# Kernel tuning notes

Measured on AMD Instinct MI355X. Metric: run time of the kernel, lower is better.

The kernel has to match this reference:

```python
import jax, jax.numpy as jnp
import numpy as np

# AmplitudeEncoder(num_modes=14, num_photons=4, UNBUNCHED, return_sv=False)
D = 1001  # math.comb(14, 4): statevector dimension


def setup_inputs() -> dict:
    key = jax.random.key(0)
    x = jax.random.normal(key, (64, 784), dtype=jnp.float32)
    return {"x": x}


def reference(x) -> jnp.ndarray:
    # flatten any trailing dims (already 2D here)
    B = x.shape[0]
    x = x.reshape(B, -1)
    F = x.shape[1]
    # pad features into a length-D statevector: state[:F] = features, rest zeros
    state = jnp.pad(x, ((0, 0), (0, D - F)))  # [B, D]
    # L2-normalize each sample's statevector (padding contributes 0 to the norm)
    state = state / jnp.linalg.norm(state, axis=1, keepdims=True)
    # density matrix: outer(state, conj(state)); input is real so conj is identity.
    # (original casts to complex128; values are identical for real features)
    return state[:, :, None] * state[:, None, :]  # [B, D, D]
```

## Files before the change

### kernel.cpp

```cpp
#include <hip/hip_runtime.h>


#define BATCH 64
#define F 784
#define D 1001
#define DD (D * D)
#define TOTAL (BATCH * DD)
#define TOTAL4 (TOTAL / 4)

typedef float vfloat4 __attribute__((ext_vector_type(4)));

__global__ __launch_bounds__(256) void amp_norm_kernel(
    const float* __restrict__ x, float* __restrict__ s) {
  const int b = blockIdx.x;
  const int t = threadIdx.x;
  const float* xb = x + b * F;

  float v0 = (t < F)       ? xb[t]       : 0.f;
  float v1 = (t + 256 < F) ? xb[t + 256] : 0.f;
  float v2 = (t + 512 < F) ? xb[t + 512] : 0.f;
  float v3 = (t + 768 < F) ? xb[t + 768] : 0.f;

  float sum = v0 * v0 + v1 * v1 + v2 * v2 + v3 * v3;

  #pragma unroll
  for (int off = 32; off > 0; off >>= 1)
    sum += __shfl_down(sum, off, 64);

  __shared__ float wsum[4];
  __shared__ float inv_s;
  const int wave = t >> 6;
  const int lane = t & 63;
  if (lane == 0) wsum[wave] = sum;
  __syncthreads();
  if (t == 0) {
    float tot = wsum[0] + wsum[1] + wsum[2] + wsum[3];
    inv_s = 1.0f / sqrtf(tot);
  }
  __syncthreads();
  const float inv = inv_s;

  float* sb = s + b * F;
  if (t < F)       sb[t]       = v0 * inv;
  if (t + 256 < F) sb[t + 256] = v1 * inv;
  if (t + 512 < F) sb[t + 512] = v2 * inv;
  if (t + 768 < F) sb[t + 768] = v3 * inv;
}

__global__ __launch_bounds__(256) void amp_outer_kernel(
    const float* __restrict__ s, float* __restrict__ out) {
  const unsigned int f4 = blockIdx.x * 256u + threadIdx.x;
  if (f4 >= (unsigned int)TOTAL4) return;
  const unsigned int f = f4 * 4u;

  unsigned int bb = f / (unsigned int)DD;
  unsigned int rem = f - bb * (unsigned int)DD;
  unsigned int ii = rem / (unsigned int)D;
  unsigned int jj = rem - ii * (unsigned int)D;

  float r = (ii < F) ? s[bb * F + ii] : 0.f;

  float vals[4];
  #pragma unroll
  for (int k = 0; k < 4; ++k) {
    float c = (jj < F) ? s[bb * F + jj] : 0.f;
    vals[k] = r * c;
    ++jj;
    if (jj == D) {
      jj = 0;
      ++ii;
      if (ii == D) { ii = 0; ++bb; }
      r = (ii < F) ? s[bb * F + ii] : 0.f;
    }
  }

  vfloat4 o = {vals[0], vals[1], vals[2], vals[3]};
  __builtin_nontemporal_store(o, (vfloat4*)(out + f));
}

extern "C" void kernel_launch(void* const* d_in, const int* in_sizes, int n_in,
                              void* d_out, int out_size, void* d_ws, size_t ws_size,
                              hipStream_t stream) {
  const float* x = (const float*)d_in[0];
  float* out = (float*)d_out;
  float* s = (float*)d_ws;

  amp_norm_kernel<<<BATCH, 256, 0, stream>>>(x, s);
  amp_outer_kernel<<<(TOTAL4 + 255) / 256, 256, 0, stream>>>(s, out);
}
```

Measured before the change: 269.3 us.

## Stage normalized rows in LDS and stream outer product with persistent blocks

The outer-product kernel now launches a fixed grid of 16 blocks per sample. Each block loads the sample's normalized vector into LDS, plus three shifted copies so unaligned columns can be read as aligned float4 vectors. Blocks then loop over float4 chunks of the output, writing zeros directly for padded rows and columns. The unaligned head and tail elements are handled separately. This removes per-element global loads and reduces index arithmetic, but it drops the nontemporal store hint and the smaller grid may reduce memory-level parallelism.

```diff
diff --git a/kernel.cpp b/kernel.cpp
--- a/kernel.cpp
+++ b/kernel.cpp
@@ -3,10 +3,10 @@
 
 #define BATCH 64
 #define F 784
-#define D 1001
-#define DD (D * D)
-#define TOTAL (BATCH * DD)
-#define TOTAL4 (TOTAL / 4)
+#define D 1001u
+#define DD 1002001u
+#define NB 16
+#define LDSW 1008
 
 typedef float vfloat4 __attribute__((ext_vector_type(4)));
 
@@ -49,33 +49,73 @@
 
 __global__ __launch_bounds__(256) void amp_outer_kernel(
     const float* __restrict__ s, float* __restrict__ out) {
-  const unsigned int f4 = blockIdx.x * 256u + threadIdx.x;
-  if (f4 >= (unsigned int)TOTAL4) return;
-  const unsigned int f = f4 * 4u;
+  __shared__ float lds[4 * LDSW];
+  const unsigned bidx = blockIdx.x;
+  const unsigned b  = bidx & 63u;
+  const unsigned nb = bidx >> 6;
+  const unsigned t  = threadIdx.x;
 
-  unsigned int bb = f / (unsigned int)DD;
-  unsigned int rem = f - bb * (unsigned int)DD;
-  unsigned int ii = rem / (unsigned int)D;
-  unsigned int jj = rem - ii * (unsigned int)D;
+  const float* sb = s + b * F;
+  for (unsigned q = t; q < LDSW; q += 256u)
+    lds[q] = (q < F) ? sb[q] : 0.f;
+  __syncthreads();
+  for (unsigned q = t; q < LDSW; q += 256u) {
+    #pragma unroll
+    for (unsigned p = 1; p < 4; ++p)
+      lds[p * LDSW + q] = (q + p < LDSW) ? lds[q + p] : 0.f;
+  }
+  __syncthreads();
 
-  float r = (ii < F) ? s[bb * F + ii] : 0.f;
+  const unsigned base = b * DD;
+  const unsigned c_lo = (base + 3u) >> 2;
+  const unsigned c_hi = (base + DD) >> 2;
+  const unsigned nch  = c_hi - c_lo;
+  const unsigned per  = (nch + (unsigned)NB - 1u) / (unsigned)NB;
+  unsigned c     = c_lo + nb * per + t;
+  unsigned c_end = c_lo + nb * per + per;
+  if (c_end > c_hi) c_end = c_hi;
 
-  float vals[4];
-  #pragma unroll
-  for (int k = 0; k < 4; ++k) {
-    float c = (jj < F) ? s[bb * F + jj] : 0.f;
-    vals[k] = r * c;
-    ++jj;
-    if (jj == D) {
-      jj = 0;
-      ++ii;
-      if (ii == D) { ii = 0; ++bb; }
-      r = (ii < F) ? s[bb * F + ii] : 0.f;
+  for (; c < c_end; c += 256u) {
+    const unsigned o = 4u * c - base;
+    const unsigned i = o / 1001u;
+    const unsigned j = o - i * 1001u;
+    vfloat4 vals;
+    if (j <= 997u) {
+      const float r = lds[i];
+      if (r != 0.f && j < 784u) {
+        const unsigned p = j & 3u;
+        const unsigned m = j & ~3u;
+        vfloat4 c4 = *(const vfloat4*)(lds + p * LDSW + m);
+        vals = c4 * r;
+      } else {
+        vals = (vfloat4){0.f, 0.f, 0.f, 0.f};
+      }
+    } else {
+      float v[4];
+      #pragma unroll
+      for (unsigned k = 0; k < 4u; ++k) {
+        unsigned jk = j + k;
+        unsigned ik = i;
+        if (jk >= 1001u) { jk -= 1001u; ik += 1u; }
+        v[k] = lds[ik] * lds[jk];
+      }
+      vals = (vfloat4){v[0], v[1], v[2], v[3]};
+    }
+    *(vfloat4*)(out + 4u * c) = vals;
+  }
+
+  if (nb == 0u) {
+    if (t == 0u) {
+      const unsigned hb = (4u - (b & 3u)) & 3u;
+      const float r0 = lds[0];
+      for (unsigned k = 0; k < hb; ++k)
+        out[base + k] = r0 * lds[k];
+    } else if (t == 1u) {
+      const unsigned tb = (b + 1u) & 3u;
+      for (unsigned k = 0; k < tb; ++k)
+        out[4u * c_hi + k] = 0.f;
     }
   }
-
-  vfloat4 o = {vals[0], vals[1], vals[2], vals[3]};
-  __builtin_nontemporal_store(o, (vfloat4*)(out + f));
 }
 
 extern "C" void kernel_launch(void* const* d_in, const int* in_sizes, int n_in,
@@ -86,5 +126,5 @@
   float* s = (float*)d_ws;
 
   amp_norm_kernel<<<BATCH, 256, 0, stream>>>(x, s);
-  amp_outer_kernel<<<(TOTAL4 + 255) / 256, 256, 0, stream>>>(s, out);
+  amp_outer_kernel<<<BATCH * NB, 256, 0, stream>>>(s, out);
 }
```

Result: faster. 254.4 us (-5.5%).
